# Kernel tuning notes

Measured on AMD Instinct MI355X. Metric: run time of the kernel, lower is better.

## Reference

```python
import jax, jax.numpy as jnp
import numpy as np

NUM_HEADS = 16
HEAD_DIM = 64
BATCH = 4
SEQ = 1024
MAX_SEQ_LEN = 2048


def _shift(pos_score):
    # Transformer-XL relative shift. pos_score: (NH, S, S_kv)
    NH, S, S_kv = pos_score.shape
    zero_pad = jnp.zeros((NH, S, 1), dtype=pos_score.dtype)
    padded = jnp.concatenate([zero_pad, pos_score], axis=-1)  # (NH, S, S_kv+1)
    padded = padded.reshape(NH, S_kv + 1, S)
    return padded[:, 1:, :].reshape(NH, S, S_kv)


def setup_inputs() -> dict:
    key = jax.random.key(0)
    ks = jax.random.split(key, 6)
    NH = BATCH * NUM_HEADS
    return {
        "queries": jax.random.normal(ks[0], (NH, SEQ, HEAD_DIM), dtype=jnp.float32),
        "keys": jax.random.normal(ks[1], (NH, SEQ, HEAD_DIM), dtype=jnp.float32),
        "values": jax.random.normal(ks[2], (NH, SEQ, HEAD_DIM), dtype=jnp.float32),
        "u_bias": jax.random.normal(ks[3], (1, NUM_HEADS, 1, HEAD_DIM), dtype=jnp.float32),
        "v_bias": jax.random.normal(ks[4], (1, NUM_HEADS, 1, HEAD_DIM), dtype=jnp.float32),
        "R": jax.random.normal(ks[5], (NUM_HEADS, MAX_SEQ_LEN, HEAD_DIM), dtype=jnp.float32),
    }


def reference(queries, keys, values, u_bias, v_bias, R):
    NH, S, d = queries.shape
    S_kv = keys.shape[1]
    batch = NH // NUM_HEADS

    q = queries * (d ** -0.5)
    q = q.reshape(batch, NUM_HEADS, S, d)
    q_u = (q + u_bias).reshape(NH, S, d)
    q_v = (q + v_bias).reshape(NH, S, d)

    # relative position embeddings, tiled over batch: (NH, S_kv, d)
    R_s = jnp.tile(R[:, :S_kv, :], (batch, 1, 1))

    content_score = jnp.einsum('nsd,ntd->nst', q_u, keys)   # (NH, S, S_kv)
    pos_score = jnp.einsum('nsd,ntd->nst', q_v, R_s)        # (NH, S, S_kv)
    pos_score = _shift(pos_score)

    attn_weights = jax.nn.softmax(content_score + pos_score, axis=-1)
    attn = jnp.einsum('nst,ntd->nsd', attn_weights, values)  # (NH, S, d)
    return attn
```

## Files before the change

kernel.cpp:

```cpp
#include <hip/hip_runtime.h>


#define SQ    1024
#define HD    64
#define NHD   16
#define RMAX  2048

typedef _Float16 f16x8 __attribute__((ext_vector_type(8)));
typedef _Float16 f16x4 __attribute__((ext_vector_type(4)));
typedef short    b16x8 __attribute__((ext_vector_type(8)));
typedef float    f32x4 __attribute__((ext_vector_type(4)));

#define MFMA_F16(A,B,C)  __builtin_amdgcn_mfma_f32_16x16x32_f16((A),(B),(C),0,0,0)
#define MFMA_BF16(A,B,C) __builtin_amdgcn_mfma_f32_16x16x32_bf16((A),(B),(C),0,0,0)

#define KH_OFF   0
#define VT_OFF   (8u << 20)
#define R16_OFF  (18u << 20)
#define WS_NEED  (20u << 20)

__device__ __forceinline__ short f2b(float f) {
  unsigned u = __builtin_bit_cast(unsigned, f);
  u += 0x7FFFu + ((u >> 16) & 1u);
  return (short)(u >> 16);
}
__device__ __forceinline__ unsigned pkh(float a, float b) {
  _Float16 h0 = (_Float16)a, h1 = (_Float16)b;
  return (unsigned)__builtin_bit_cast(unsigned short, h0)
       | ((unsigned)__builtin_bit_cast(unsigned short, h1) << 16);
}
__device__ __forceinline__ unsigned pkb(float a, float b) {
  return (unsigned)(unsigned short)f2b(a)
       | ((unsigned)(unsigned short)f2b(b) << 16);
}


__global__ __launch_bounds__(256) void preprep(
    const float* __restrict__ K, const float* __restrict__ R,
    const float* __restrict__ V,
    _Float16* __restrict__ Kh, _Float16* __restrict__ R16,
    short* __restrict__ Vt)
{
  __shared__ float t[64][65];
  const int bid = blockIdx.x, tid = threadIdx.x;
  if (bid < 1024) {
    const int n = bid >> 4, st = bid & 15;
    {
      const int row = tid >> 2, c0 = (tid & 3) * 16;
      const float* src = V + ((size_t)n * SQ + st * 64 + row) * HD + c0;
#pragma unroll
      for (int i = 0; i < 4; ++i) {
        float4 x = ((const float4*)src)[i];
        t[row][c0 + 4*i + 0] = x.x; t[row][c0 + 4*i + 1] = x.y;
        t[row][c0 + 4*i + 2] = x.z; t[row][c0 + 4*i + 3] = x.w;
      }
    }
    __syncthreads();
    {
      const int d = tid >> 2, s0 = (tid & 3) * 16;
      short* dst = Vt + ((size_t)n * 80 + d) * SQ + st * 64 + s0;
#pragma unroll
      for (int i = 0; i < 8; ++i)
        *(unsigned*)(dst + 2*i) = pkb(t[s0 + 2*i][d], t[s0 + 2*i + 1][d]);
    }
    if (tid < 64) {
      const int s = st * 64 + tid;
      Vt[((size_t)n * 80 + 64) * SQ + s] = (short)0x3F80;
#pragma unroll
      for (int r = 65; r < 80; ++r) Vt[((size_t)n * 80 + r) * SQ + s] = 0;
    }
  } else {
    const int idx = (bid - 1024) * 256 + tid;
    const int nk4 = (64 * SQ * HD) / 4;
    if (idx < nk4) {
      float4 v = ((const float4*)K)[idx];
      f16x4 o = { (_Float16)v.x, (_Float16)v.y, (_Float16)v.z, (_Float16)v.w };
      *(f16x4*)(Kh + 4 * (size_t)idx) = o;
    } else {
      int rr = idx - nk4;
      int h  = rr >> 14, off = rr & 16383;
      float4 v = ((const float4*)R)[((size_t)h << 15) + off];
      f16x4 o = { (_Float16)v.x, (_Float16)v.y, (_Float16)v.z, (_Float16)v.w };
      *(f16x4*)(R16 + 4 * (((size_t)h << 14) + off)) = o;
    }
  }
}


__global__ __launch_bounds__(256, 4) void relpos_sdpa_r7(
    const float* __restrict__ Q, const _Float16* __restrict__ Kh,
    const short* __restrict__ Vtg, const _Float16* __restrict__ R16,
    const float* __restrict__ Ub, const float* __restrict__ Vb,
    float* __restrict__ O)
{
  const int n    = blockIdx.x;
  const int h    = n & (NHD - 1);
  const int a0   = blockIdx.y * 64;
  const int tid  = threadIdx.x;
  const int lane = tid & 63, wave = tid >> 6;
  const int l15  = lane & 15, quad = lane >> 4;

  const float*    Qn  = Q   + (size_t)n * SQ * HD;
  const _Float16* Khn = Kh  + (size_t)n * SQ * HD;
  const short*    Vgn = Vtg + (size_t)n * 80 * SQ;
  const _Float16* Rh  = R16 + (size_t)h * SQ * HD;

  __shared__ __align__(16) char lds[38160];
  _Float16* Kb  = (_Float16*)lds;
  unsigned short* Ps = (unsigned short*)lds;
  short*    Vt  = (short*)(lds + 9216);
  unsigned* Pb2 = (unsigned*)(lds + 9216 + 11520);
  const _Float16* Pb2h = (const _Float16*)Pb2;

  f16x8 quF[2], qvF[5][2];
#pragma unroll
  for (int ks = 0; ks < 2; ++ks) {
    const int db = ks * 32 + quad * 8;
    float ub[8], vb[8];
#pragma unroll
    for (int j = 0; j < 8; ++j) { ub[j] = Ub[h*HD + db + j]; vb[j] = Vb[h*HD + db + j]; }
    {
      const float* p = Qn + (size_t)(a0 + 16*wave + l15) * HD + db;
      f16x8 f;
#pragma unroll
      for (int j = 0; j < 8; ++j) f[j] = (_Float16)(p[j] * 0.125f + ub[j]);
      quF[ks] = f;
    }
#pragma unroll
    for (int rt = 0; rt < 5; ++rt) {
      int row = a0 + 16*rt + l15; if (row > SQ-1) row = SQ-1;
      const float* p = Qn + (size_t)row * HD + db;
      f16x8 f;
#pragma unroll
      for (int j = 0; j < 8; ++j) f[j] = (_Float16)(p[j] * 0.125f + vb[j]);
      qvF[rt][ks] = f;
    }
  }

  if (tid < 64) Vt[64*72 + tid] = (short)0x3F80;

  f32x4 Oacc[5];
#pragma unroll
  for (int ct = 0; ct < 5; ++ct) Oacc[ct] = (f32x4){0.f, 0.f, 0.f, 0.f};

  auto band = [&](int jstart) {
    const int c    = jstart + 16*wave + l15;
    const int j    = (c + 2048) & (SQ - 1);
    const int slot = (c + 2048) & 127;
    const _Float16* rp = Rh + (size_t)j * HD + quad * 8;
    f16x8 B0 = *(const f16x8*)rp;
    f16x8 B1 = *(const f16x8*)(rp + 32);
#pragma unroll
    for (int rt = 0; rt < 5; ++rt) {
      f32x4 acc = (f32x4){0.f, 0.f, 0.f, 0.f};
      acc = MFMA_F16(qvF[rt][0], B0, acc);
      acc = MFMA_F16(qvF[rt][1], B1, acc);
      if (rt < 4) {
        const int rp0 = 8*rt + 2*quad;
        Pb2[rp0*132 + slot]       = pkh(acc[0], acc[1]);
        Pb2[(rp0 + 1)*132 + slot] = pkh(acc[2], acc[3]);
      } else if (quad == 0) {
        Pb2[32*132 + slot] = pkh(acc[0], acc[1]);
      }
    }
  };

  band(-a0 - 65);
  band(-a0 - 1);

  const int sr = tid >> 2, sc4 = tid & 3;
  const int iiB = 16*wave + 4*quad;

  for (int k0 = 0; k0 < SQ; k0 += 64) {
    __syncthreads();

    {
      const _Float16* src = Khn + (size_t)(k0 + sr) * HD + sc4 * 16;
      *(f16x8*)&Kb[sr*72 + sc4*16]     = *(const f16x8*)src;
      *(f16x8*)&Kb[sr*72 + sc4*16 + 8] = *(const f16x8*)(src + 8);
    }
    {
      const short* src = Vgn + (size_t)sr * SQ + k0 + sc4 * 16;
      *(b16x8*)&Vt[sr*72 + sc4*16]     = *(const b16x8*)src;
      *(b16x8*)&Vt[sr*72 + sc4*16 + 8] = *(const b16x8*)(src + 8);
    }
    __syncthreads();

    f32x4 sc[4];
#pragma unroll
    for (int ct = 0; ct < 4; ++ct) {
      f16x8 b0 = *(const f16x8*)&Kb[(16*ct + l15)*72 + quad*8];
      f16x8 b1 = *(const f16x8*)&Kb[(16*ct + l15)*72 + 32 + quad*8];
      f32x4 acc = (f32x4){0.f, 0.f, 0.f, 0.f};
      acc = MFMA_F16(quF[0], b0, acc);
      acc = MFMA_F16(quF[1], b1, acc);
      sc[ct] = acc;
    }

    const int dlt = k0 - a0;
#pragma unroll
    for (int r = 0; r < 4; ++r) {
      const int ii = iiB + r;
      const int adA = (ii >> 1) * 264 + (ii & 1);
      const int adB = ((ii + 1) >> 1) * 264 + ((ii + 1) & 1);
#pragma unroll
      for (int ct = 0; ct < 4; ++ct) {
        const int e    = dlt + 16*ct + l15 - ii;
        const int u    = (e > 0) ? 1 : 0;
        const int slot = (e - 1 - u) & 127;
        float pos = (float)Pb2h[(u ? adB : adA) + 2*slot];
        float s   = sc[ct][r] + ((e == 1) ? 0.f : pos);
        sc[ct][r] = __expf(s - 40.0f);
      }
    }
    __syncthreads();

#pragma unroll
    for (int r = 0; r < 4; ++r) {
      unsigned w0 = pkb(sc[0][r], sc[1][r]);
      unsigned w1 = pkb(sc[2][r], sc[3][r]);
      const int pbase = (iiB + r)*68 + l15;
      Ps[pbase]      = (unsigned short)w0;
      Ps[pbase + 16] = (unsigned short)(w0 >> 16);
      Ps[pbase + 32] = (unsigned short)w1;
      Ps[pbase + 48] = (unsigned short)(w1 >> 16);
    }

    b16x8 pA0 = *(const b16x8*)&Ps[(16*wave + l15)*68 + quad*8];
    b16x8 pA1 = *(const b16x8*)&Ps[(16*wave + l15)*68 + 32 + quad*8];
#pragma unroll
    for (int ct = 0; ct < 5; ++ct) {
      b16x8 v0 = *(const b16x8*)&Vt[(16*ct + l15)*72 + quad*8];
      b16x8 v1 = *(const b16x8*)&Vt[(16*ct + l15)*72 + 32 + quad*8];
      Oacc[ct] = MFMA_BF16(pA0, v0, Oacc[ct]);
      Oacc[ct] = MFMA_BF16(pA1, v1, Oacc[ct]);
    }

    if (k0 < SQ - 64) band(k0 + 64 - a0 - 1);
  }

#pragma unroll
  for (int r = 0; r < 4; ++r) {
    float l   = __shfl(Oacc[4][r], lane & 48);
    float inv = 1.0f / l;
    const size_t rowo = (size_t)n * SQ * HD + (size_t)(a0 + iiB + r) * HD;
#pragma unroll
    for (int ct = 0; ct < 4; ++ct)
      O[rowo + 16*ct + l15] = Oacc[ct][r] * inv;
  }
}


__global__ __launch_bounds__(256, 4) void relpos_sdpa_fb(
    const float* __restrict__ Q, const float* __restrict__ K,
    const float* __restrict__ V, const float* __restrict__ Ub,
    const float* __restrict__ Vb, const float* __restrict__ R,
    float* __restrict__ O)
{
  const int n    = blockIdx.x;
  const int h    = n & (NHD - 1);
  const int a0   = blockIdx.y * 64;
  const int tid  = threadIdx.x;
  const int lane = tid & 63, wave = tid >> 6;
  const int l15  = lane & 15, quad = lane >> 4;

  const float* Qn = Q + (size_t)n * SQ * HD;
  const float* Kn = K + (size_t)n * SQ * HD;
  const float* Vn = V + (size_t)n * SQ * HD;
  const float* Rh = R + (size_t)h * RMAX * HD;

  __shared__ __align__(16) char lds[38656];
  _Float16* Kb = (_Float16*)lds;
  short*    Ps = (short*)lds;
  short*    Vt = (short*)(lds + 9216);
  _Float16* Pb = (_Float16*)(lds + 9216 + 11520);

  f16x8 quF[2], qvF[5][2];
#pragma unroll
  for (int ks = 0; ks < 2; ++ks) {
    const int db = ks * 32 + quad * 8;
    float ub[8], vb[8];
#pragma unroll
    for (int j = 0; j < 8; ++j) { ub[j] = Ub[h*HD + db + j]; vb[j] = Vb[h*HD + db + j]; }
    {
      const float* p = Qn + (size_t)(a0 + 16*wave + l15) * HD + db;
      f16x8 f;
#pragma unroll
      for (int j = 0; j < 8; ++j) f[j] = (_Float16)(p[j] * 0.125f + ub[j]);
      quF[ks] = f;
    }
#pragma unroll
    for (int rt = 0; rt < 5; ++rt) {
      int row = a0 + 16*rt + l15; if (row > SQ-1) row = SQ-1;
      const float* p = Qn + (size_t)row * HD + db;
      f16x8 f;
#pragma unroll
      for (int j = 0; j < 8; ++j) f[j] = (_Float16)(p[j] * 0.125f + vb[j]);
      qvF[rt][ks] = f;
    }
  }

  if (tid < 64) Vt[64*72 + tid] = (short)0x3F80;

  f32x4 Oacc[5];
#pragma unroll
  for (int ct = 0; ct < 5; ++ct) Oacc[ct] = (f32x4){0.f, 0.f, 0.f, 0.f};

  auto band = [&](int jstart) {
    const int c    = jstart + 16*wave + l15;
    const int j    = (c + 2048) & (SQ - 1);
    const int slot = (c + 2048) & 127;
    const float* rp = Rh + (size_t)j * HD + quad * 8;
    f16x8 B0, B1;
    {
      float4 x0 = *(const float4*)(rp),      x1 = *(const float4*)(rp + 4);
      float4 y0 = *(const float4*)(rp + 32), y1 = *(const float4*)(rp + 36);
#pragma unroll
      for (int t = 0; t < 4; ++t) { B0[t] = (_Float16)(&x0.x)[t]; B0[t+4] = (_Float16)(&x1.x)[t]; }
#pragma unroll
      for (int t = 0; t < 4; ++t) { B1[t] = (_Float16)(&y0.x)[t]; B1[t+4] = (_Float16)(&y1.x)[t]; }
    }
#pragma unroll
    for (int rt = 0; rt < 5; ++rt) {
      f32x4 acc = (f32x4){0.f, 0.f, 0.f, 0.f};
      acc = MFMA_F16(qvF[rt][0], B0, acc);
      acc = MFMA_F16(qvF[rt][1], B1, acc);
      const int row = 16*rt + 4*quad;
      if (rt < 4) {
        *(unsigned*)&Pb[slot*70 + row]     = pkh(acc[0], acc[1]);
        *(unsigned*)&Pb[slot*70 + row + 2] = pkh(acc[2], acc[3]);
      } else if (quad == 0) {
        *(unsigned*)&Pb[slot*70 + row]     = pkh(acc[0], acc[1]);
      }
    }
  };

  band(-a0 - 65);
  band(-a0 - 1);

  const int sr = tid >> 2, sc4 = tid & 3;
  const int iiB = 16*wave + 4*quad;

  for (int k0 = 0; k0 < SQ; k0 += 64) {
    __syncthreads();
    {
      const float* src = Kn + (size_t)(k0 + sr) * HD + sc4 * 16;
      float4 x0 = *(const float4*)(src),     x1 = *(const float4*)(src + 4);
      float4 y0 = *(const float4*)(src + 8), y1 = *(const float4*)(src + 12);
      f16x8 lo, hi;
#pragma unroll
      for (int t = 0; t < 4; ++t) { lo[t] = (_Float16)(&x0.x)[t]; lo[t+4] = (_Float16)(&x1.x)[t]; }
#pragma unroll
      for (int t = 0; t < 4; ++t) { hi[t] = (_Float16)(&y0.x)[t]; hi[t+4] = (_Float16)(&y1.x)[t]; }
      *(f16x8*)&Kb[sr*72 + sc4*16]     = lo;
      *(f16x8*)&Kb[sr*72 + sc4*16 + 8] = hi;
    }
    {
      const int g = lane >> 3;
#pragma unroll
      for (int i = 0; i < 8; ++i) {
        int bp = 8*wave + (i ^ g);
        float v0 = Vn[(size_t)(k0 + 2*bp)     * HD + lane];
        float v1 = Vn[(size_t)(k0 + 2*bp + 1) * HD + lane];
        *(unsigned*)&Vt[lane*72 + 2*bp] = pkb(v0, v1);
      }
    }
    __syncthreads();

    f32x4 sc[4];
#pragma unroll
    for (int ct = 0; ct < 4; ++ct) {
      f16x8 b0 = *(const f16x8*)&Kb[(16*ct + l15)*72 + quad*8];
      f16x8 b1 = *(const f16x8*)&Kb[(16*ct + l15)*72 + 32 + quad*8];
      f32x4 acc = (f32x4){0.f, 0.f, 0.f, 0.f};
      acc = MFMA_F16(quF[0], b0, acc);
      acc = MFMA_F16(quF[1], b1, acc);
      sc[ct] = acc;
    }

    const int dlt = k0 - a0;
#pragma unroll
    for (int r = 0; r < 4; ++r) {
      const int ii = iiB + r;
#pragma unroll
      for (int ct = 0; ct < 4; ++ct) {
        const int e    = dlt + 16*ct + l15 - ii;
        const int u    = (e > 0) ? 1 : 0;
        const int slot = (e - 1 - u + 2048) & 127;
        float pos = (float)Pb[slot*70 + ii + u];
        float s   = sc[ct][r] + ((e == 1) ? 0.f : pos);
        sc[ct][r] = __expf(s - 40.0f);
      }
    }
    __syncthreads();

#pragma unroll
    for (int r = 0; r < 4; ++r)
#pragma unroll
      for (int ct = 0; ct < 4; ++ct)
        Ps[(iiB + r)*68 + 16*ct + l15] = f2b(sc[ct][r]);

    b16x8 pA0 = *(const b16x8*)&Ps[(16*wave + l15)*68 + quad*8];
    b16x8 pA1 = *(const b16x8*)&Ps[(16*wave + l15)*68 + 32 + quad*8];
#pragma unroll
    for (int ct = 0; ct < 5; ++ct) {
      b16x8 v0 = *(const b16x8*)&Vt[(16*ct + l15)*72 + quad*8];
      b16x8 v1 = *(const b16x8*)&Vt[(16*ct + l15)*72 + 32 + quad*8];
      Oacc[ct] = MFMA_BF16(pA0, v0, Oacc[ct]);
      Oacc[ct] = MFMA_BF16(pA1, v1, Oacc[ct]);
    }

    if (k0 < SQ - 64) band(k0 + 64 - a0 - 1);
  }

#pragma unroll
  for (int r = 0; r < 4; ++r) {
    float l   = __shfl(Oacc[4][r], lane & 48);
    float inv = 1.0f / l;
    const size_t rowo = (size_t)n * SQ * HD + (size_t)(a0 + iiB + r) * HD;
#pragma unroll
    for (int ct = 0; ct < 4; ++ct)
      O[rowo + 16*ct + l15] = Oacc[ct][r] * inv;
  }
}

extern "C" void kernel_launch(void* const* d_in, const int* in_sizes, int n_in,
                              void* d_out, int out_size, void* d_ws, size_t ws_size,
                              hipStream_t stream) {
  const float* Q  = (const float*)d_in[0];
  const float* K  = (const float*)d_in[1];
  const float* V  = (const float*)d_in[2];
  const float* Ub = (const float*)d_in[3];
  const float* Vb = (const float*)d_in[4];
  const float* R  = (const float*)d_in[5];
  float* O = (float*)d_out;

  if (ws_size >= WS_NEED) {
    _Float16* Kh  = (_Float16*)((char*)d_ws + KH_OFF);
    short*    Vt  = (short*)((char*)d_ws + VT_OFF);
    _Float16* R16 = (_Float16*)((char*)d_ws + R16_OFF);

    preprep<<<6144, 256, 0, stream>>>(K, R, V, Kh, R16, Vt);

    dim3 grid(64, 16);
    relpos_sdpa_r7<<<grid, 256, 0, stream>>>(Q, Kh, Vt, R16, Ub, Vb, O);
  } else {
    dim3 grid(64, 16);
    relpos_sdpa_fb<<<grid, 256, 0, stream>>>(Q, K, V, Ub, Vb, R, O);
  }
}
```

Measured before the change: 189.9 us.

## Drop fp16/bf16 preconversion kernel and convert K, V, R inline in one kernel

Removes the separate preprep kernel that converted K, R and transposed V into fp16/bf16 workspace buffers, and instead launches a single fused kernel that converts from fp32 while staging tiles into LDS. It also folds log2(e) into the query scaling so the softmax uses a native exp2. It switches bf16 packing to a cheaper round-half-up form and adopts a transposed, padded layout for the positional-score band buffer. This saves one launch and the workspace round trip, at the cost of reading fp32 K/V/R (twice the bytes) repeatedly across the 16 query tiles.

```diff
diff --git a/kernel.cpp b/kernel.cpp
--- a/kernel.cpp
+++ b/kernel.cpp
@@ -7,251 +7,35 @@
 #define RMAX  2048
 
 typedef _Float16 f16x8 __attribute__((ext_vector_type(8)));
-typedef _Float16 f16x4 __attribute__((ext_vector_type(4)));
 typedef short    b16x8 __attribute__((ext_vector_type(8)));
 typedef float    f32x4 __attribute__((ext_vector_type(4)));
 
 #define MFMA_F16(A,B,C)  __builtin_amdgcn_mfma_f32_16x16x32_f16((A),(B),(C),0,0,0)
 #define MFMA_BF16(A,B,C) __builtin_amdgcn_mfma_f32_16x16x32_bf16((A),(B),(C),0,0,0)
 
-#define KH_OFF   0
-#define VT_OFF   (8u << 20)
-#define R16_OFF  (18u << 20)
-#define WS_NEED  (20u << 20)
-
-__device__ __forceinline__ short f2b(float f) {
-  unsigned u = __builtin_bit_cast(unsigned, f);
-  u += 0x7FFFu + ((u >> 16) & 1u);
-  return (short)(u >> 16);
+#define L2E 1.44269504088896f
+#define QS  (0.125f * L2E)
+
+__device__ __forceinline__ float exp2fast(float x) {
+#if __has_builtin(__builtin_amdgcn_exp2f)
+  return __builtin_amdgcn_exp2f(x);
+#else
+  return __expf(x * 0.693147180559945f);
+#endif
+}
+
+__device__ __forceinline__ unsigned pkb2(float a, float b) {
+  unsigned ua = __builtin_bit_cast(unsigned, a) + 0x8000u;
+  unsigned ub = __builtin_bit_cast(unsigned, b) + 0x8000u;
+  return (ub & 0xFFFF0000u) | (ua >> 16);
 }
 __device__ __forceinline__ unsigned pkh(float a, float b) {
   _Float16 h0 = (_Float16)a, h1 = (_Float16)b;
   return (unsigned)__builtin_bit_cast(unsigned short, h0)
        | ((unsigned)__builtin_bit_cast(unsigned short, h1) << 16);
 }
-__device__ __forceinline__ unsigned pkb(float a, float b) {
-  return (unsigned)(unsigned short)f2b(a)
-       | ((unsigned)(unsigned short)f2b(b) << 16);
-}
-
-
-__global__ __launch_bounds__(256) void preprep(
-    const float* __restrict__ K, const float* __restrict__ R,
-    const float* __restrict__ V,
-    _Float16* __restrict__ Kh, _Float16* __restrict__ R16,
-    short* __restrict__ Vt)
-{
-  __shared__ float t[64][65];
-  const int bid = blockIdx.x, tid = threadIdx.x;
-  if (bid < 1024) {
-    const int n = bid >> 4, st = bid & 15;
-    {
-      const int row = tid >> 2, c0 = (tid & 3) * 16;
-      const float* src = V + ((size_t)n * SQ + st * 64 + row) * HD + c0;
-#pragma unroll
-      for (int i = 0; i < 4; ++i) {
-        float4 x = ((const float4*)src)[i];
-        t[row][c0 + 4*i + 0] = x.x; t[row][c0 + 4*i + 1] = x.y;
-        t[row][c0 + 4*i + 2] = x.z; t[row][c0 + 4*i + 3] = x.w;
-      }
-    }
-    __syncthreads();
-    {
-      const int d = tid >> 2, s0 = (tid & 3) * 16;
-      short* dst = Vt + ((size_t)n * 80 + d) * SQ + st * 64 + s0;
-#pragma unroll
-      for (int i = 0; i < 8; ++i)
-        *(unsigned*)(dst + 2*i) = pkb(t[s0 + 2*i][d], t[s0 + 2*i + 1][d]);
-    }
-    if (tid < 64) {
-      const int s = st * 64 + tid;
-      Vt[((size_t)n * 80 + 64) * SQ + s] = (short)0x3F80;
-#pragma unroll
-      for (int r = 65; r < 80; ++r) Vt[((size_t)n * 80 + r) * SQ + s] = 0;
-    }
-  } else {
-    const int idx = (bid - 1024) * 256 + tid;
-    const int nk4 = (64 * SQ * HD) / 4;
-    if (idx < nk4) {
-      float4 v = ((const float4*)K)[idx];
-      f16x4 o = { (_Float16)v.x, (_Float16)v.y, (_Float16)v.z, (_Float16)v.w };
-      *(f16x4*)(Kh + 4 * (size_t)idx) = o;
-    } else {
-      int rr = idx - nk4;
-      int h  = rr >> 14, off = rr & 16383;
-      float4 v = ((const float4*)R)[((size_t)h << 15) + off];
-      f16x4 o = { (_Float16)v.x, (_Float16)v.y, (_Float16)v.z, (_Float16)v.w };
-      *(f16x4*)(R16 + 4 * (((size_t)h << 14) + off)) = o;
-    }
-  }
-}
-
-
-__global__ __launch_bounds__(256, 4) void relpos_sdpa_r7(
-    const float* __restrict__ Q, const _Float16* __restrict__ Kh,
-    const short* __restrict__ Vtg, const _Float16* __restrict__ R16,
-    const float* __restrict__ Ub, const float* __restrict__ Vb,
-    float* __restrict__ O)
-{
-  const int n    = blockIdx.x;
-  const int h    = n & (NHD - 1);
-  const int a0   = blockIdx.y * 64;
-  const int tid  = threadIdx.x;
-  const int lane = tid & 63, wave = tid >> 6;
-  const int l15  = lane & 15, quad = lane >> 4;
-
-  const float*    Qn  = Q   + (size_t)n * SQ * HD;
-  const _Float16* Khn = Kh  + (size_t)n * SQ * HD;
-  const short*    Vgn = Vtg + (size_t)n * 80 * SQ;
-  const _Float16* Rh  = R16 + (size_t)h * SQ * HD;
-
-  __shared__ __align__(16) char lds[38160];
-  _Float16* Kb  = (_Float16*)lds;
-  unsigned short* Ps = (unsigned short*)lds;
-  short*    Vt  = (short*)(lds + 9216);
-  unsigned* Pb2 = (unsigned*)(lds + 9216 + 11520);
-  const _Float16* Pb2h = (const _Float16*)Pb2;
-
-  f16x8 quF[2], qvF[5][2];
-#pragma unroll
-  for (int ks = 0; ks < 2; ++ks) {
-    const int db = ks * 32 + quad * 8;
-    float ub[8], vb[8];
-#pragma unroll
-    for (int j = 0; j < 8; ++j) { ub[j] = Ub[h*HD + db + j]; vb[j] = Vb[h*HD + db + j]; }
-    {
-      const float* p = Qn + (size_t)(a0 + 16*wave + l15) * HD + db;
-      f16x8 f;
-#pragma unroll
-      for (int j = 0; j < 8; ++j) f[j] = (_Float16)(p[j] * 0.125f + ub[j]);
-      quF[ks] = f;
-    }
-#pragma unroll
-    for (int rt = 0; rt < 5; ++rt) {
-      int row = a0 + 16*rt + l15; if (row > SQ-1) row = SQ-1;
-      const float* p = Qn + (size_t)row * HD + db;
-      f16x8 f;
-#pragma unroll
-      for (int j = 0; j < 8; ++j) f[j] = (_Float16)(p[j] * 0.125f + vb[j]);
-      qvF[rt][ks] = f;
-    }
-  }
-
-  if (tid < 64) Vt[64*72 + tid] = (short)0x3F80;
-
-  f32x4 Oacc[5];
-#pragma unroll
-  for (int ct = 0; ct < 5; ++ct) Oacc[ct] = (f32x4){0.f, 0.f, 0.f, 0.f};
-
-  auto band = [&](int jstart) {
-    const int c    = jstart + 16*wave + l15;
-    const int j    = (c + 2048) & (SQ - 1);
-    const int slot = (c + 2048) & 127;
-    const _Float16* rp = Rh + (size_t)j * HD + quad * 8;
-    f16x8 B0 = *(const f16x8*)rp;
-    f16x8 B1 = *(const f16x8*)(rp + 32);
-#pragma unroll
-    for (int rt = 0; rt < 5; ++rt) {
-      f32x4 acc = (f32x4){0.f, 0.f, 0.f, 0.f};
-      acc = MFMA_F16(qvF[rt][0], B0, acc);
-      acc = MFMA_F16(qvF[rt][1], B1, acc);
-      if (rt < 4) {
-        const int rp0 = 8*rt + 2*quad;
-        Pb2[rp0*132 + slot]       = pkh(acc[0], acc[1]);
-        Pb2[(rp0 + 1)*132 + slot] = pkh(acc[2], acc[3]);
-      } else if (quad == 0) {
-        Pb2[32*132 + slot] = pkh(acc[0], acc[1]);
-      }
-    }
-  };
-
-  band(-a0 - 65);
-  band(-a0 - 1);
-
-  const int sr = tid >> 2, sc4 = tid & 3;
-  const int iiB = 16*wave + 4*quad;
-
-  for (int k0 = 0; k0 < SQ; k0 += 64) {
-    __syncthreads();
-
-    {
-      const _Float16* src = Khn + (size_t)(k0 + sr) * HD + sc4 * 16;
-      *(f16x8*)&Kb[sr*72 + sc4*16]     = *(const f16x8*)src;
-      *(f16x8*)&Kb[sr*72 + sc4*16 + 8] = *(const f16x8*)(src + 8);
-    }
-    {
-      const short* src = Vgn + (size_t)sr * SQ + k0 + sc4 * 16;
-      *(b16x8*)&Vt[sr*72 + sc4*16]     = *(const b16x8*)src;
-      *(b16x8*)&Vt[sr*72 + sc4*16 + 8] = *(const b16x8*)(src + 8);
-    }
-    __syncthreads();
-
-    f32x4 sc[4];
-#pragma unroll
-    for (int ct = 0; ct < 4; ++ct) {
-      f16x8 b0 = *(const f16x8*)&Kb[(16*ct + l15)*72 + quad*8];
-      f16x8 b1 = *(const f16x8*)&Kb[(16*ct + l15)*72 + 32 + quad*8];
-      f32x4 acc = (f32x4){0.f, 0.f, 0.f, 0.f};
-      acc = MFMA_F16(quF[0], b0, acc);
-      acc = MFMA_F16(quF[1], b1, acc);
-      sc[ct] = acc;
-    }
-
-    const int dlt = k0 - a0;
-#pragma unroll
-    for (int r = 0; r < 4; ++r) {
-      const int ii = iiB + r;
-      const int adA = (ii >> 1) * 264 + (ii & 1);
-      const int adB = ((ii + 1) >> 1) * 264 + ((ii + 1) & 1);
-#pragma unroll
-      for (int ct = 0; ct < 4; ++ct) {
-        const int e    = dlt + 16*ct + l15 - ii;
-        const int u    = (e > 0) ? 1 : 0;
-        const int slot = (e - 1 - u) & 127;
-        float pos = (float)Pb2h[(u ? adB : adA) + 2*slot];
-        float s   = sc[ct][r] + ((e == 1) ? 0.f : pos);
-        sc[ct][r] = __expf(s - 40.0f);
-      }
-    }
-    __syncthreads();
-
-#pragma unroll
-    for (int r = 0; r < 4; ++r) {
-      unsigned w0 = pkb(sc[0][r], sc[1][r]);
-      unsigned w1 = pkb(sc[2][r], sc[3][r]);
-      const int pbase = (iiB + r)*68 + l15;
-      Ps[pbase]      = (unsigned short)w0;
-      Ps[pbase + 16] = (unsigned short)(w0 >> 16);
-      Ps[pbase + 32] = (unsigned short)w1;
-      Ps[pbase + 48] = (unsigned short)(w1 >> 16);
-    }
-
-    b16x8 pA0 = *(const b16x8*)&Ps[(16*wave + l15)*68 + quad*8];
-    b16x8 pA1 = *(const b16x8*)&Ps[(16*wave + l15)*68 + 32 + quad*8];
-#pragma unroll
-    for (int ct = 0; ct < 5; ++ct) {
-      b16x8 v0 = *(const b16x8*)&Vt[(16*ct + l15)*72 + quad*8];
-      b16x8 v1 = *(const b16x8*)&Vt[(16*ct + l15)*72 + 32 + quad*8];
-      Oacc[ct] = MFMA_BF16(pA0, v0, Oacc[ct]);
-      Oacc[ct] = MFMA_BF16(pA1, v1, Oacc[ct]);
-    }
-
-    if (k0 < SQ - 64) band(k0 + 64 - a0 - 1);
-  }
-
-#pragma unroll
-  for (int r = 0; r < 4; ++r) {
-    float l   = __shfl(Oacc[4][r], lane & 48);
-    float inv = 1.0f / l;
-    const size_t rowo = (size_t)n * SQ * HD + (size_t)(a0 + iiB + r) * HD;
-#pragma unroll
-    for (int ct = 0; ct < 4; ++ct)
-      O[rowo + 16*ct + l15] = Oacc[ct][r] * inv;
-  }
-}
-
-
-__global__ __launch_bounds__(256, 4) void relpos_sdpa_fb(
+
+__global__ __launch_bounds__(256, 4) void relpos_sdpa_r8(
     const float* __restrict__ Q, const float* __restrict__ K,
     const float* __restrict__ V, const float* __restrict__ Ub,
     const float* __restrict__ Vb, const float* __restrict__ R,
@@ -269,11 +53,12 @@
   const float* Vn = V + (size_t)n * SQ * HD;
   const float* Rh = R + (size_t)h * RMAX * HD;
 
-  __shared__ __align__(16) char lds[38656];
-  _Float16* Kb = (_Float16*)lds;
-  short*    Ps = (short*)lds;
-  short*    Vt = (short*)(lds + 9216);
-  _Float16* Pb = (_Float16*)(lds + 9216 + 11520);
+  __shared__ __align__(16) char lds[38424];
+  _Float16* Kb  = (_Float16*)lds;
+  unsigned short* Ps = (unsigned short*)lds;
+  short*    Vt  = (short*)(lds + 9216);
+  unsigned* Pb2 = (unsigned*)(lds + 9216 + 11520);
+  const _Float16* Pb2h = (const _Float16*)Pb2;
 
   f16x8 quF[2], qvF[5][2];
 #pragma unroll
@@ -281,26 +66,41 @@
     const int db = ks * 32 + quad * 8;
     float ub[8], vb[8];
 #pragma unroll
-    for (int j = 0; j < 8; ++j) { ub[j] = Ub[h*HD + db + j]; vb[j] = Vb[h*HD + db + j]; }
+    for (int j = 0; j < 8; ++j) {
+      ub[j] = Ub[h*HD + db + j] * L2E;
+      vb[j] = Vb[h*HD + db + j] * L2E;
+    }
     {
       const float* p = Qn + (size_t)(a0 + 16*wave + l15) * HD + db;
+      float4 x0 = ((const float4*)p)[0], x1 = ((const float4*)p)[1];
       f16x8 f;
 #pragma unroll
-      for (int j = 0; j < 8; ++j) f[j] = (_Float16)(p[j] * 0.125f + ub[j]);
+      for (int t = 0; t < 4; ++t) {
+        f[t]   = (_Float16)((&x0.x)[t] * QS + ub[t]);
+        f[t+4] = (_Float16)((&x1.x)[t] * QS + ub[t+4]);
+      }
       quF[ks] = f;
     }
 #pragma unroll
     for (int rt = 0; rt < 5; ++rt) {
       int row = a0 + 16*rt + l15; if (row > SQ-1) row = SQ-1;
       const float* p = Qn + (size_t)row * HD + db;
+      float4 x0 = ((const float4*)p)[0], x1 = ((const float4*)p)[1];
       f16x8 f;
 #pragma unroll
-      for (int j = 0; j < 8; ++j) f[j] = (_Float16)(p[j] * 0.125f + vb[j]);
+      for (int t = 0; t < 4; ++t) {
+        f[t]   = (_Float16)((&x0.x)[t] * QS + vb[t]);
+        f[t+4] = (_Float16)((&x1.x)[t] * QS + vb[t+4]);
+      }
       qvF[rt][ks] = f;
     }
   }
 
-  if (tid < 64) Vt[64*72 + tid] = (short)0x3F80;
+  if (tid < 64) {
+    Vt[64*72 + tid] = (short)0x3F80;
+#pragma unroll
+    for (int r2 = 65; r2 < 80; ++r2) Vt[r2*72 + tid] = 0;
+  }
 
   f32x4 Oacc[5];
 #pragma unroll
@@ -311,26 +111,24 @@
     const int j    = (c + 2048) & (SQ - 1);
     const int slot = (c + 2048) & 127;
     const float* rp = Rh + (size_t)j * HD + quad * 8;
+    float4 x0 = *(const float4*)(rp),      x1 = *(const float4*)(rp + 4);
+    float4 y0 = *(const float4*)(rp + 32), y1 = *(const float4*)(rp + 36);
     f16x8 B0, B1;
-    {
-      float4 x0 = *(const float4*)(rp),      x1 = *(const float4*)(rp + 4);
-      float4 y0 = *(const float4*)(rp + 32), y1 = *(const float4*)(rp + 36);
-#pragma unroll
-      for (int t = 0; t < 4; ++t) { B0[t] = (_Float16)(&x0.x)[t]; B0[t+4] = (_Float16)(&x1.x)[t]; }
-#pragma unroll
-      for (int t = 0; t < 4; ++t) { B1[t] = (_Float16)(&y0.x)[t]; B1[t+4] = (_Float16)(&y1.x)[t]; }
-    }
+#pragma unroll
+    for (int t = 0; t < 4; ++t) { B0[t] = (_Float16)(&x0.x)[t]; B0[t+4] = (_Float16)(&x1.x)[t]; }
+#pragma unroll
+    for (int t = 0; t < 4; ++t) { B1[t] = (_Float16)(&y0.x)[t]; B1[t+4] = (_Float16)(&y1.x)[t]; }
 #pragma unroll
     for (int rt = 0; rt < 5; ++rt) {
       f32x4 acc = (f32x4){0.f, 0.f, 0.f, 0.f};
       acc = MFMA_F16(qvF[rt][0], B0, acc);
       acc = MFMA_F16(qvF[rt][1], B1, acc);
-      const int row = 16*rt + 4*quad;
       if (rt < 4) {
-        *(unsigned*)&Pb[slot*70 + row]     = pkh(acc[0], acc[1]);
-        *(unsigned*)&Pb[slot*70 + row + 2] = pkh(acc[2], acc[3]);
+        const int rp0 = 8*rt + 2*quad;
+        Pb2[rp0*134 + slot]       = pkh(acc[0], acc[1]);
+        Pb2[(rp0 + 1)*134 + slot] = pkh(acc[2], acc[3]);
       } else if (quad == 0) {
-        *(unsigned*)&Pb[slot*70 + row]     = pkh(acc[0], acc[1]);
+        Pb2[32*134 + slot] = pkh(acc[0], acc[1]);
       }
     }
   };
@@ -339,30 +137,31 @@
   band(-a0 - 1);
 
   const int sr = tid >> 2, sc4 = tid & 3;
+  const int g8 = lane >> 3;
   const int iiB = 16*wave + 4*quad;
 
   for (int k0 = 0; k0 < SQ; k0 += 64) {
     __syncthreads();
+
     {
       const float* src = Kn + (size_t)(k0 + sr) * HD + sc4 * 16;
-      float4 x0 = *(const float4*)(src),     x1 = *(const float4*)(src + 4);
-      float4 y0 = *(const float4*)(src + 8), y1 = *(const float4*)(src + 12);
+      float4 x0 = ((const float4*)src)[0], x1 = ((const float4*)src)[1];
+      float4 x2 = ((const float4*)src)[2], x3 = ((const float4*)src)[3];
       f16x8 lo, hi;
 #pragma unroll
       for (int t = 0; t < 4; ++t) { lo[t] = (_Float16)(&x0.x)[t]; lo[t+4] = (_Float16)(&x1.x)[t]; }
 #pragma unroll
-      for (int t = 0; t < 4; ++t) { hi[t] = (_Float16)(&y0.x)[t]; hi[t+4] = (_Float16)(&y1.x)[t]; }
+      for (int t = 0; t < 4; ++t) { hi[t] = (_Float16)(&x2.x)[t]; hi[t+4] = (_Float16)(&x3.x)[t]; }
       *(f16x8*)&Kb[sr*72 + sc4*16]     = lo;
       *(f16x8*)&Kb[sr*72 + sc4*16 + 8] = hi;
     }
     {
-      const int g = lane >> 3;
 #pragma unroll
       for (int i = 0; i < 8; ++i) {
-        int bp = 8*wave + (i ^ g);
+        int bp = 8*wave + (i ^ g8);
         float v0 = Vn[(size_t)(k0 + 2*bp)     * HD + lane];
         float v1 = Vn[(size_t)(k0 + 2*bp + 1) * HD + lane];
-        *(unsigned*)&Vt[lane*72 + 2*bp] = pkb(v0, v1);
+        *(unsigned*)&Vt[lane*72 + 2*bp] = pkb2(v0, v1);
       }
     }
     __syncthreads();
@@ -382,23 +181,30 @@
 #pragma unroll
     for (int r = 0; r < 4; ++r) {
       const int ii = iiB + r;
+      const int adA = (ii >> 1) * 268 + (ii & 1);
+      const int adB = ((ii + 1) >> 1) * 268 + ((ii + 1) & 1);
 #pragma unroll
       for (int ct = 0; ct < 4; ++ct) {
         const int e    = dlt + 16*ct + l15 - ii;
         const int u    = (e > 0) ? 1 : 0;
-        const int slot = (e - 1 - u + 2048) & 127;
-        float pos = (float)Pb[slot*70 + ii + u];
+        const int slot = (e - 1 - u) & 127;
+        float pos = (float)Pb2h[(u ? adB : adA) + 2*slot];
         float s   = sc[ct][r] + ((e == 1) ? 0.f : pos);
-        sc[ct][r] = __expf(s - 40.0f);
+        sc[ct][r] = exp2fast(s - 57.7078016f);
       }
     }
     __syncthreads();
 
 #pragma unroll
-    for (int r = 0; r < 4; ++r)
-#pragma unroll
-      for (int ct = 0; ct < 4; ++ct)
-        Ps[(iiB + r)*68 + 16*ct + l15] = f2b(sc[ct][r]);
+    for (int r = 0; r < 4; ++r) {
+      unsigned w0 = pkb2(sc[0][r], sc[1][r]);
+      unsigned w1 = pkb2(sc[2][r], sc[3][r]);
+      const int pbase = (iiB + r)*68 + l15;
+      Ps[pbase]      = (unsigned short)w0;
+      Ps[pbase + 16] = (unsigned short)(w0 >> 16);
+      Ps[pbase + 32] = (unsigned short)w1;
+      Ps[pbase + 48] = (unsigned short)(w1 >> 16);
+    }
 
     b16x8 pA0 = *(const b16x8*)&Ps[(16*wave + l15)*68 + quad*8];
     b16x8 pA1 = *(const b16x8*)&Ps[(16*wave + l15)*68 + 32 + quad*8];
@@ -435,17 +241,7 @@
   const float* R  = (const float*)d_in[5];
   float* O = (float*)d_out;
 
-  if (ws_size >= WS_NEED) {
-    _Float16* Kh  = (_Float16*)((char*)d_ws + KH_OFF);
-    short*    Vt  = (short*)((char*)d_ws + VT_OFF);
-    _Float16* R16 = (_Float16*)((char*)d_ws + R16_OFF);
-
-    preprep<<<6144, 256, 0, stream>>>(K, R, V, Kh, R16, Vt);
-
-    dim3 grid(64, 16);
-    relpos_sdpa_r7<<<grid, 256, 0, stream>>>(Q, Kh, Vt, R16, Ub, Vb, O);
-  } else {
-    dim3 grid(64, 16);
-    relpos_sdpa_fb<<<grid, 256, 0, stream>>>(Q, K, V, Ub, Vb, R, O);
-  }
-}
+  (void)d_ws; (void)ws_size;
+  dim3 grid(64, 16);
+  relpos_sdpa_r8<<<grid, 256, 0, stream>>>(Q, K, V, Ub, Vb, R, O);
+}
```

Measured after the change: 227.4 us. 1.2x slower.

## Prefetch K/V tiles in registers, ring-buffer band writes, fold log2e into Q

Applied to the files above, without the earlier changes.

Global loads for the next K/V tile now go into registers one iteration ahead and are written to LDS at the top of the loop, so their latency overlaps compute. Band results are held in registers and written to the positional ring after the barrier, and the P buffer gets its own LDS region, which removes one __syncthreads per iteration. log2e is folded into the Q scaling so exp2 replaces exp, and the bf16 packing switches to a cheaper round-half-up. Costs are a larger LDS footprint (about 47KB versus 38KB), which may lower occupancy, more registers held live, and slightly different rounding.

```diff
diff --git a/kernel.cpp b/kernel.cpp
--- a/kernel.cpp
+++ b/kernel.cpp
@@ -14,11 +14,21 @@
 #define MFMA_F16(A,B,C)  __builtin_amdgcn_mfma_f32_16x16x32_f16((A),(B),(C),0,0,0)
 #define MFMA_BF16(A,B,C) __builtin_amdgcn_mfma_f32_16x16x32_bf16((A),(B),(C),0,0,0)
 
+#define L2E 1.44269504088896f
+
 #define KH_OFF   0
 #define VT_OFF   (8u << 20)
 #define R16_OFF  (18u << 20)
 #define WS_NEED  (20u << 20)
 
+__device__ __forceinline__ float exp2fast(float x) {
+#if __has_builtin(__builtin_amdgcn_exp2f)
+  return __builtin_amdgcn_exp2f(x);
+#else
+  return __expf(x * 0.693147180559945f);
+#endif
+}
+
 __device__ __forceinline__ short f2b(float f) {
   unsigned u = __builtin_bit_cast(unsigned, f);
   u += 0x7FFFu + ((u >> 16) & 1u);
@@ -29,9 +39,10 @@
   return (unsigned)__builtin_bit_cast(unsigned short, h0)
        | ((unsigned)__builtin_bit_cast(unsigned short, h1) << 16);
 }
-__device__ __forceinline__ unsigned pkb(float a, float b) {
-  return (unsigned)(unsigned short)f2b(a)
-       | ((unsigned)(unsigned short)f2b(b) << 16);
+__device__ __forceinline__ unsigned pkb2(float a, float b) {
+  unsigned ua = __builtin_bit_cast(unsigned, a) + 0x8000u;
+  unsigned ub = __builtin_bit_cast(unsigned, b) + 0x8000u;
+  return (ub & 0xFFFF0000u) | (ua >> 16);
 }
 
 
@@ -61,7 +72,7 @@
       short* dst = Vt + ((size_t)n * 80 + d) * SQ + st * 64 + s0;
 #pragma unroll
       for (int i = 0; i < 8; ++i)
-        *(unsigned*)(dst + 2*i) = pkb(t[s0 + 2*i][d], t[s0 + 2*i + 1][d]);
+        *(unsigned*)(dst + 2*i) = pkb2(t[s0 + 2*i][d], t[s0 + 2*i + 1][d]);
     }
     if (tid < 64) {
       const int s = st * 64 + tid;
@@ -87,7 +98,7 @@
 }
 
 
-__global__ __launch_bounds__(256, 4) void relpos_sdpa_r7(
+__global__ __launch_bounds__(256, 4) void relpos_sdpa_r9(
     const float* __restrict__ Q, const _Float16* __restrict__ Kh,
     const short* __restrict__ Vtg, const _Float16* __restrict__ R16,
     const float* __restrict__ Ub, const float* __restrict__ Vb,
@@ -105,11 +116,11 @@
   const short*    Vgn = Vtg + (size_t)n * 80 * SQ;
   const _Float16* Rh  = R16 + (size_t)h * SQ * HD;
 
-  __shared__ __align__(16) char lds[38160];
-  _Float16* Kb  = (_Float16*)lds;
-  unsigned short* Ps = (unsigned short*)lds;
-  short*    Vt  = (short*)(lds + 9216);
-  unsigned* Pb2 = (unsigned*)(lds + 9216 + 11520);
+  __shared__ __align__(16) char lds[47128];
+  _Float16*       Kb  = (_Float16*)lds;
+  short*          Vt  = (short*)(lds + 9216);
+  unsigned short* Ps  = (unsigned short*)(lds + 9216 + 11520);
+  unsigned*       Pb2 = (unsigned*)(lds + 9216 + 11520 + 8704);
   const _Float16* Pb2h = (const _Float16*)Pb2;
 
   f16x8 quF[2], qvF[5][2];
@@ -118,21 +129,32 @@
     const int db = ks * 32 + quad * 8;
     float ub[8], vb[8];
 #pragma unroll
-    for (int j = 0; j < 8; ++j) { ub[j] = Ub[h*HD + db + j]; vb[j] = Vb[h*HD + db + j]; }
+    for (int j = 0; j < 8; ++j) {
+      ub[j] = Ub[h*HD + db + j] * L2E;
+      vb[j] = Vb[h*HD + db + j] * L2E;
+    }
     {
       const float* p = Qn + (size_t)(a0 + 16*wave + l15) * HD + db;
+      float4 x0 = ((const float4*)p)[0], x1 = ((const float4*)p)[1];
       f16x8 f;
 #pragma unroll
-      for (int j = 0; j < 8; ++j) f[j] = (_Float16)(p[j] * 0.125f + ub[j]);
+      for (int t = 0; t < 4; ++t) {
+        f[t]   = (_Float16)((&x0.x)[t] * (0.125f * L2E) + ub[t]);
+        f[t+4] = (_Float16)((&x1.x)[t] * (0.125f * L2E) + ub[t+4]);
+      }
       quF[ks] = f;
     }
 #pragma unroll
     for (int rt = 0; rt < 5; ++rt) {
       int row = a0 + 16*rt + l15; if (row > SQ-1) row = SQ-1;
       const float* p = Qn + (size_t)row * HD + db;
+      float4 x0 = ((const float4*)p)[0], x1 = ((const float4*)p)[1];
       f16x8 f;
 #pragma unroll
-      for (int j = 0; j < 8; ++j) f[j] = (_Float16)(p[j] * 0.125f + vb[j]);
+      for (int t = 0; t < 4; ++t) {
+        f[t]   = (_Float16)((&x0.x)[t] * (0.125f * L2E) + vb[t]);
+        f[t+4] = (_Float16)((&x1.x)[t] * (0.125f * L2E) + vb[t+4]);
+      }
       qvF[rt][ks] = f;
     }
   }
@@ -143,10 +165,12 @@
 #pragma unroll
   for (int ct = 0; ct < 5; ++ct) Oacc[ct] = (f32x4){0.f, 0.f, 0.f, 0.f};
 
+  unsigned ringW[9];
+  int ringSlot;
   auto band = [&](int jstart) {
     const int c    = jstart + 16*wave + l15;
     const int j    = (c + 2048) & (SQ - 1);
-    const int slot = (c + 2048) & 127;
+    ringSlot       = (c + 2048) & 127;
     const _Float16* rp = Rh + (size_t)j * HD + quad * 8;
     f16x8 B0 = *(const f16x8*)rp;
     f16x8 B1 = *(const f16x8*)(rp + 32);
@@ -156,35 +180,55 @@
       acc = MFMA_F16(qvF[rt][0], B0, acc);
       acc = MFMA_F16(qvF[rt][1], B1, acc);
       if (rt < 4) {
-        const int rp0 = 8*rt + 2*quad;
-        Pb2[rp0*132 + slot]       = pkh(acc[0], acc[1]);
-        Pb2[(rp0 + 1)*132 + slot] = pkh(acc[2], acc[3]);
-      } else if (quad == 0) {
-        Pb2[32*132 + slot] = pkh(acc[0], acc[1]);
+        ringW[2*rt]     = pkh(acc[0], acc[1]);
+        ringW[2*rt + 1] = pkh(acc[2], acc[3]);
+      } else {
+        ringW[8] = pkh(acc[0], acc[1]);
       }
     }
   };
-
-  band(-a0 - 65);
-  band(-a0 - 1);
-
-  const int sr = tid >> 2, sc4 = tid & 3;
+  auto ringFlush = [&]() {
+#pragma unroll
+    for (int rt = 0; rt < 4; ++rt) {
+      const int rp0 = 8*rt + 2*quad;
+      Pb2[rp0*134 + ringSlot]       = ringW[2*rt];
+      Pb2[(rp0 + 1)*134 + ringSlot] = ringW[2*rt + 1];
+    }
+    if (quad == 0) Pb2[32*134 + ringSlot] = ringW[8];
+  };
+
+  band(-a0 - 65);  ringFlush();
+  band(-a0 - 1);   ringFlush();
+
+  f16x8 kPre[2]; b16x8 vPre[2];
+  auto stageLoad = [&](int k0) {
+    const _Float16* ks = Khn + (size_t)(k0 + lane) * HD + wave*8;
+    kPre[0] = *(const f16x8*)ks;
+    kPre[1] = *(const f16x8*)(ks + 32);
+    const short* vs = Vgn + (size_t)lane * SQ + k0 + wave*8;
+    vPre[0] = *(const b16x8*)vs;
+    vPre[1] = *(const b16x8*)(vs + 32);
+  };
+  auto stageWrite = [&]() {
+    *(f16x8*)&Kb[lane*72 + wave*8]      = kPre[0];
+    *(f16x8*)&Kb[lane*72 + wave*8 + 32] = kPre[1];
+    *(b16x8*)&Vt[lane*72 + wave*8]      = vPre[0];
+    *(b16x8*)&Vt[lane*72 + wave*8 + 32] = vPre[1];
+  };
+
+  stageLoad(0);
+
   const int iiB = 16*wave + 4*quad;
 
   for (int k0 = 0; k0 < SQ; k0 += 64) {
     __syncthreads();
 
-    {
-      const _Float16* src = Khn + (size_t)(k0 + sr) * HD + sc4 * 16;
-      *(f16x8*)&Kb[sr*72 + sc4*16]     = *(const f16x8*)src;
-      *(f16x8*)&Kb[sr*72 + sc4*16 + 8] = *(const f16x8*)(src + 8);
-    }
-    {
-      const short* src = Vgn + (size_t)sr * SQ + k0 + sc4 * 16;
-      *(b16x8*)&Vt[sr*72 + sc4*16]     = *(const b16x8*)src;
-      *(b16x8*)&Vt[sr*72 + sc4*16 + 8] = *(const b16x8*)(src + 8);
-    }
-    __syncthreads();
+    stageWrite();
+    if (k0 > 0) ringFlush();
+
+    __syncthreads();
+
+    if (k0 < SQ - 64) stageLoad(k0 + 64);
 
     f32x4 sc[4];
 #pragma unroll
@@ -201,8 +245,8 @@
 #pragma unroll
     for (int r = 0; r < 4; ++r) {
       const int ii = iiB + r;
-      const int adA = (ii >> 1) * 264 + (ii & 1);
-      const int adB = ((ii + 1) >> 1) * 264 + ((ii + 1) & 1);
+      const int adA = (ii >> 1) * 268 + (ii & 1);
+      const int adB = ((ii + 1) >> 1) * 268 + ((ii + 1) & 1);
 #pragma unroll
       for (int ct = 0; ct < 4; ++ct) {
         const int e    = dlt + 16*ct + l15 - ii;
@@ -210,15 +254,14 @@
         const int slot = (e - 1 - u) & 127;
         float pos = (float)Pb2h[(u ? adB : adA) + 2*slot];
         float s   = sc[ct][r] + ((e == 1) ? 0.f : pos);
-        sc[ct][r] = __expf(s - 40.0f);
-      }
-    }
-    __syncthreads();
+        sc[ct][r] = exp2fast(s - 57.7078016f);
+      }
+    }
 
 #pragma unroll
     for (int r = 0; r < 4; ++r) {
-      unsigned w0 = pkb(sc[0][r], sc[1][r]);
-      unsigned w1 = pkb(sc[2][r], sc[3][r]);
+      unsigned w0 = pkb2(sc[0][r], sc[1][r]);
+      unsigned w1 = pkb2(sc[2][r], sc[3][r]);
       const int pbase = (iiB + r)*68 + l15;
       Ps[pbase]      = (unsigned short)w0;
       Ps[pbase + 16] = (unsigned short)(w0 >> 16);
@@ -362,7 +405,7 @@
         int bp = 8*wave + (i ^ g);
         float v0 = Vn[(size_t)(k0 + 2*bp)     * HD + lane];
         float v1 = Vn[(size_t)(k0 + 2*bp + 1) * HD + lane];
-        *(unsigned*)&Vt[lane*72 + 2*bp] = pkb(v0, v1);
+        *(unsigned*)&Vt[lane*72 + 2*bp] = pkb2(v0, v1);
       }
     }
     __syncthreads();
@@ -443,7 +486,7 @@
     preprep<<<6144, 256, 0, stream>>>(K, R, V, Kh, R16, Vt);
 
     dim3 grid(64, 16);
-    relpos_sdpa_r7<<<grid, 256, 0, stream>>>(Q, Kh, Vt, R16, Ub, Vb, O);
+    relpos_sdpa_r9<<<grid, 256, 0, stream>>>(Q, Kh, Vt, R16, Ub, Vb, O);
   } else {
     dim3 grid(64, 16);
     relpos_sdpa_fb<<<grid, 256, 0, stream>>>(Q, K, V, Ub, Vb, R, O);
```

Measured after the change: 196.9 us. 3.7% more time.
